# Performance work log

Measured on AMD Instinct MI355X. Metric: run time of the kernel, lower is better.

Reference implementation:

```python
import jax, jax.numpy as jnp
import numpy as np

G, NPG = 2048, 512          # glimpses, points per glimpse
N0 = G * NPG                # 1,048,576 input points
CPG, CPG2 = 128, 32         # clusters per glimpse at level1/level2
M1, M2 = G * CPG, G * CPG2  # 262144, 65536


def _seg_mean_np(x, ids, m):
    cnt = np.bincount(ids, minlength=m).astype(np.float32)
    out = np.stack([np.bincount(ids, weights=x[:, d], minlength=m) for d in range(x.shape[1])], axis=1)
    return (out / np.maximum(cnt, 1.0)[:, None]).astype(np.float32)


def setup_inputs() -> dict:
    key = jax.random.key(0)
    ks = jax.random.split(key, 16)
    rng = np.random.default_rng(0)
    pos_np = (rng.random((N0, 3)) * 4.0).astype(np.float32)
    # voxel_mean_pool level 0: each point -> a cluster within its glimpse
    g_of_pt = np.arange(N0) // NPG
    out_index0 = (g_of_pt * CPG + rng.integers(0, CPG, N0)).astype(np.int64)
    pos1_np = _seg_mean_np(pos_np, out_index0, M1)
    g_of_c1 = np.arange(M1) // CPG
    out_index1 = (g_of_c1 * CPG2 + rng.integers(0, CPG2, M1)).astype(np.int64)
    pos2_np = _seg_mean_np(pos1_np, out_index1, M2)
    out_index2 = (np.arange(M2) // CPG2).astype(np.int64)  # glimpse id per level-2 point

    def w(k, shp, s=0.05):
        return jax.random.normal(k, shp, dtype=jnp.float32) * s

    return {
        "rgb": jax.random.normal(ks[0], (N0, 1), dtype=jnp.float32),
        "pos": jnp.asarray(pos_np), "pos1": jnp.asarray(pos1_np), "pos2": jnp.asarray(pos2_np),
        "out_index0": jnp.asarray(out_index0), "out_index1": jnp.asarray(out_index1),
        "out_index2": jnp.asarray(out_index2),
        "eps": jax.random.normal(ks[1], (G, 128), dtype=jnp.float32),
        # conv1: local (c_in=1 + 3 -> 16), global (16 -> 32)
        "W1l": w(ks[2], (4, 16)), "b1l": jnp.zeros(16), "W1g": w(ks[3], (16, 32)), "b1g": jnp.zeros(32),
        # conv2: (32+3 -> 64), (64 -> 128)
        "W2l": w(ks[4], (35, 64)), "b2l": jnp.zeros(64), "W2g": w(ks[5], (64, 128)), "b2g": jnp.zeros(128),
        # conv3: (128+3 -> 128), (128 -> 256)
        "W3l": w(ks[6], (131, 128)), "b3l": jnp.zeros(128), "W3g": w(ks[7], (128, 256)), "b3g": jnp.zeros(256),
        "Wlin": w(ks[8], (256, 256)), "blin": jnp.zeros(256),
    }


def _point_conv(x_in, pos_in, pos_out, out_index, Wl, bl, Wg, bg):
    # gather relative position of each input point w.r.t. its output center
    rel = pos_in - pos_out[out_index]                      # [E,3]
    h = jax.nn.celu(jnp.concatenate([x_in, rel], -1) @ Wl + bl)  # per-edge MLP
    m = pos_out.shape[0]
    cnt = jax.ops.segment_sum(jnp.ones((h.shape[0],), h.dtype), out_index, num_segments=m)
    agg = jax.ops.segment_sum(h, out_index, num_segments=m) / jnp.maximum(cnt, 1.0)[:, None]
    return agg @ Wg + bg


def reference(rgb, pos, pos1, pos2, out_index0, out_index1, out_index2, eps,
              W1l, b1l, W1g, b1g, W2l, b2l, W2g, b2g, W3l, b3l, W3g, b3g, Wlin, blin):
    f = rgb  # ar=False path: feature = rgb
    f = jax.nn.celu(_point_conv(f, pos, pos1, out_index0, W1l, b1l, W1g, b1g))   # [M1,32]
    f = jax.nn.celu(_point_conv(f, pos1, pos2, out_index1, W2l, b2l, W2g, b2g))  # [M2,128]
    centers = jnp.zeros((G, 3), f.dtype)  # pos_sample = zeros_like(glimpse__center)
    f = jax.nn.celu(_point_conv(f, pos2, centers, out_index2, W3l, b3l, W3g, b3g))  # [G,256]
    out = f @ Wlin + blin
    mu, sg = jnp.split(out, 2, axis=1)
    sigma = jax.nn.softplus(sg)  # to_sigma
    z = mu + sigma * eps         # Normal.rsample
    z_what, z_mask = jnp.split(z, 2, axis=1)
    return z_what, z_mask, mu, sigma, f
```

## Files before the change

kernel.cpp:

```cpp
#include <hip/hip_runtime.h>
#include <hip/hip_bf16.h>
#include <cstddef>

#define G_   2048
#define NPG_ 512
#define CPG_ 128
#define CPG2_ 32
#define N0_  (G_*NPG_)
#define M1_  (G_*CPG_)
#define M2_  (G_*CPG2_)

#define OFF_ZW 0
#define OFF_ZM (G_*64)
#define OFF_MU (2*G_*64)
#define OFF_SG (2*G_*64 + G_*128)
#define OFF_F  (2*G_*64 + 2*G_*128)

typedef __attribute__((ext_vector_type(8))) short bf16x8;
typedef __attribute__((ext_vector_type(4))) float f32x4;

__device__ __forceinline__ float celu_f(float x)     { return x > 0.f ? x : __expf(x) - 1.f; }
__device__ __forceinline__ float softplus_f(float x) { return fmaxf(x, 0.f) + __logf(1.f + __expf(-fabsf(x))); }
__device__ __forceinline__ unsigned short f2bf(float x) {
    __hip_bfloat16 h = __float2bfloat16(x);
    return *reinterpret_cast<unsigned short*>(&h);
}

__global__ __launch_bounds__(256, 6) void k_conv1(
    const float* __restrict__ rgb, const float* __restrict__ pos, const float* __restrict__ pos1,
    const int* __restrict__ idx0, const float* __restrict__ W1l, const float* __restrict__ b1l,
    const float* __restrict__ W1g, const float* __restrict__ b1g, unsigned short* __restrict__ f1,
    const float* __restrict__ W2l, const float* __restrict__ W2g, const float* __restrict__ W3l,
    const float* __restrict__ W3g, const float* __restrict__ Wlin,
    unsigned short* __restrict__ w2lT, unsigned short* __restrict__ w2gT,
    unsigned short* __restrict__ w3lT, unsigned short* __restrict__ w3gT,
    unsigned short* __restrict__ wlinT)
{
    const int g = blockIdx.x, t = threadIdx.x;

    {
        const size_t tid = (size_t)g*256 + t, stride = (size_t)gridDim.x*256;
        for (size_t i = tid; i < 64*64; i += stride) {
            const int ch = i >> 6, k = i & 63;
            w2lT[i] = f2bf(k < 35 ? W2l[k*64 + ch] : 0.f);
        }
        for (size_t i = tid; i < 128*64; i += stride) {
            const int ch = i >> 6, k = i & 63;
            w2gT[i] = f2bf(W2g[k*128 + ch]);
        }
        for (size_t i = tid; i < 128*160; i += stride) {
            const int ch = i / 160, k = i % 160;
            w3lT[i] = f2bf(k < 131 ? W3l[k*128 + ch] : 0.f);
        }
        for (size_t i = tid; i < 256*128; i += stride) {
            const int ch = i >> 7, k = i & 127;
            w3gT[i] = f2bf(W3g[k*256 + ch]);
        }
        for (size_t i = tid; i < 256*256; i += stride) {
            const int ch = i >> 8, k = i & 255;
            wlinT[i] = f2bf(Wlin[k*256 + ch]);
        }
    }

    __shared__ float sx0[NPG_], srx[NPG_], sry[NPG_], srz[NPG_];
    __shared__ unsigned short slc1[NPG_], order[NPG_];
    __shared__ int cnt[CPG_], start[CPG_], ctr[CPG_], scan[CPG_];
    __shared__ float aggT[CPG_*20];
    __shared__ float sW1g[512];

    for (int i = t; i < 512; i += 256) sW1g[i] = W1g[i];
    if (t < CPG_) cnt[t] = 0;
    __syncthreads();

    #pragma unroll
    for (int r = 0; r < 2; r++) {
        const int lp = r*256 + t;
        const int p  = g*NPG_ + lp;
        const int c  = idx0[p];
        const int lc = c - g*CPG_;
        sx0[lp] = rgb[p];
        srx[lp] = pos[p*3+0] - pos1[c*3+0];
        sry[lp] = pos[p*3+1] - pos1[c*3+1];
        srz[lp] = pos[p*3+2] - pos1[c*3+2];
        slc1[lp] = (unsigned short)lc;
        atomicAdd(&cnt[lc], 1);
    }
    __syncthreads();

    if (t < CPG_) {
        int val = cnt[t];
        const int ln = t & 63;
        #pragma unroll
        for (int d = 1; d < 64; d <<= 1) {
            const int v = __shfl_up(val, d, 64);
            if (ln >= d) val += v;
        }
        scan[t] = val;
    }
    __syncthreads();
    if (t >= 64 && t < CPG_) scan[t] += scan[63];
    __syncthreads();
    if (t < CPG_) { const int s = scan[t] - cnt[t]; start[t] = s; ctr[t] = s; }
    __syncthreads();

    #pragma unroll
    for (int r = 0; r < 2; r++) {
        const int lp = r*256 + t;
        const int slot = atomicAdd(&ctr[slc1[lp]], 1);
        order[slot] = (unsigned short)lp;
    }
    __syncthreads();

    {
        const int c = t >> 1, ch0 = (t & 1) * 8;
        float wj[8], wx[8], wy[8], wz[8], bb2[8];
        #pragma unroll
        for (int j = 0; j < 8; j++) {
            wj[j] = W1l[ch0+j]; wx[j] = W1l[16+ch0+j];
            wy[j] = W1l[32+ch0+j]; wz[j] = W1l[48+ch0+j];
            bb2[j] = b1l[ch0+j];
        }
        float a[8];
        #pragma unroll
        for (int j = 0; j < 8; j++) a[j] = 0.f;
        const int n = cnt[c], base = start[c];
        for (int i = 0; i < n; i++) {
            const int lp = order[base + i];
            const float x0 = sx0[lp], rx = srx[lp], ry = sry[lp], rz = srz[lp];
            #pragma unroll
            for (int j = 0; j < 8; j++) {
                const float h = bb2[j] + x0*wj[j] + rx*wx[j] + ry*wy[j] + rz*wz[j];
                a[j] += celu_f(h);
            }
        }
        const float inv = 1.f / fmaxf((float)n, 1.f);
        #pragma unroll
        for (int j = 0; j < 8; j++) aggT[c*20 + ch0 + j] = a[j] * inv;
    }
    __syncthreads();

    const int oc = t & 31;
    float wreg[16];
    #pragma unroll
    for (int j = 0; j < 16; j++) wreg[j] = sW1g[j*32 + oc];
    const float bg = b1g[oc];
    #pragma unroll
    for (int i = 0; i < 16; i++) {
        const int lc = (t >> 5) + i*8;
        float a = bg;
        #pragma unroll
        for (int j = 0; j < 16; j += 4) {
            const float4 a4 = *(const float4*)&aggT[lc*20 + j];
            a += a4.x*wreg[j] + a4.y*wreg[j+1] + a4.z*wreg[j+2] + a4.w*wreg[j+3];
        }
        f1[(size_t)(g*CPG_ + lc)*32 + oc] = f2bf(celu_f(a));
    }
}

__global__ __launch_bounds__(256, 5) void k_conv2(
    const unsigned short* __restrict__ f1, const float* __restrict__ pos1, const float* __restrict__ pos2,
    const int* __restrict__ idx1, const unsigned short* __restrict__ w2lT, const float* __restrict__ b2l,
    const unsigned short* __restrict__ w2gT, const float* __restrict__ b2g, unsigned short* __restrict__ f2)
{
    const int g = blockIdx.x, t = threadIdx.x;
    const int lane = t & 63, wv = t >> 6;
    const int lr = lane & 15, quad = lane >> 4;
    __shared__ __align__(16) unsigned short xs16[CPG_*72];
    __shared__ __align__(16) unsigned short sT[32*136];
    __shared__ int   slc[CPG_];
    __shared__ int   cnti[CPG2_];
    __shared__ float invc[CPG2_];
    unsigned short* const HT   = sT - 0 + 0, *const HT_unused = nullptr;
    unsigned short* const HTp  = xs16;
    unsigned short* const agg2 = sT;

    for (int i = t; i < 1088; i += 256) ((uint2*)sT)[i] = make_uint2(0u, 0u);
    if (t < CPG2_) cnti[t] = 0;
    {
        const uint4 v0 = ((const uint4*)f1)[(size_t)g*512 + t*2];
        const uint4 v1 = ((const uint4*)f1)[(size_t)g*512 + t*2 + 1];
        const int row = t >> 1, col = (t & 1) * 16;
        *(uint4*)&xs16[row*72 + col]     = v0;
        *(uint4*)&xs16[row*72 + col + 8] = v1;
    }
    for (int i = t; i < 128*29; i += 256) {
        const int r = i / 29, c = 35 + (i - r*29);
        xs16[r*72 + c] = 0;
    }
    if (t < CPG_) {
        const int c2 = idx1[g*CPG_ + t];
        slc[t] = c2 - g*CPG2_;
        #pragma unroll
        for (int d = 0; d < 3; d++)
            xs16[t*72 + 32 + d] = f2bf(pos1[(g*CPG_ + t)*3 + d] - pos2[c2*3 + d]);
    }
    __syncthreads();

    float hv[8][4];
    {
        const int chn = wv*16 + lr;
        const bf16x8 bw0 = *(const bf16x8*)&w2lT[chn*64 + quad*8];
        const bf16x8 bw1 = *(const bf16x8*)&w2lT[chn*64 + 32 + quad*8];
        const float bias = b2l[chn];
        #pragma unroll
        for (int m = 0; m < 8; m++) {
            f32x4 acc = (f32x4){bias, bias, bias, bias};
            const bf16x8 a0 = *(const bf16x8*)&xs16[(m*16 + lr)*72 + quad*8];
            const bf16x8 a1 = *(const bf16x8*)&xs16[(m*16 + lr)*72 + 32 + quad*8];
            acc = __builtin_amdgcn_mfma_f32_16x16x32_bf16(a0, bw0, acc, 0, 0, 0);
            acc = __builtin_amdgcn_mfma_f32_16x16x32_bf16(a1, bw1, acc, 0, 0, 0);
            #pragma unroll
            for (int r = 0; r < 4; r++) hv[m][r] = celu_f(acc[r]);
        }
    }
    if (t < CPG_) {
        sT[slc[t]*136 + t] = 0x3F80;
        atomicAdd(&cnti[slc[t]], 1);
    }
    __syncthreads();

    {
        const int chn = wv*16 + lr;
        #pragma unroll
        for (int m = 0; m < 8; m++) {
            uint2 p;
            p.x = (unsigned)f2bf(hv[m][0]) | ((unsigned)f2bf(hv[m][1]) << 16);
            p.y = (unsigned)f2bf(hv[m][2]) | ((unsigned)f2bf(hv[m][3]) << 16);
            *(uint2*)&HTp[chn*136 + m*16 + quad*4] = p;
        }
    }
    if (t < CPG2_) invc[t] = 1.f / fmaxf((float)cnti[t], 1.f);
    __syncthreads();

    float aggv[2][4];
    {
        const int ch = wv*16 + lr;
        f32x4 acc[2];
        acc[0] = (f32x4){0.f, 0.f, 0.f, 0.f};
        acc[1] = (f32x4){0.f, 0.f, 0.f, 0.f};
        #pragma unroll
        for (int ks = 0; ks < 4; ks++) {
            const bf16x8 b = *(const bf16x8*)&HTp[ch*136 + ks*32 + quad*8];
            #pragma unroll
            for (int mt = 0; mt < 2; mt++) {
                const bf16x8 a = *(const bf16x8*)&sT[(mt*16 + lr)*136 + ks*32 + quad*8];
                acc[mt] = __builtin_amdgcn_mfma_f32_16x16x32_bf16(a, b, acc[mt], 0, 0, 0);
            }
        }
        #pragma unroll
        for (int mt = 0; mt < 2; mt++)
        #pragma unroll
        for (int r = 0; r < 4; r++) {
            const int s = mt*16 + quad*4 + r;
            aggv[mt][r] = acc[mt][r] * invc[s];
        }
    }
    __syncthreads();

    {
        const int ch = wv*16 + lr;
        #pragma unroll
        for (int mt = 0; mt < 2; mt++)
        #pragma unroll
        for (int r = 0; r < 4; r++)
            agg2[(mt*16 + quad*4 + r)*72 + ch] = f2bf(aggv[mt][r]);
    }
    __syncthreads();

    {
        f32x4 acc2[2][2];
        int   chn2[2];
        bf16x8 bw[2][2];
        #pragma unroll
        for (int nt = 0; nt < 2; nt++) {
            chn2[nt] = (wv + nt*4)*16 + lr;
            const float bias = b2g[chn2[nt]];
            #pragma unroll
            for (int mt = 0; mt < 2; mt++) acc2[nt][mt] = (f32x4){bias, bias, bias, bias};
            bw[nt][0] = *(const bf16x8*)&w2gT[chn2[nt]*64 + quad*8];
            bw[nt][1] = *(const bf16x8*)&w2gT[chn2[nt]*64 + 32 + quad*8];
        }
        #pragma unroll
        for (int ks = 0; ks < 2; ks++) {
            #pragma unroll
            for (int mt = 0; mt < 2; mt++) {
                const bf16x8 a = *(const bf16x8*)&agg2[(mt*16 + lr)*72 + ks*32 + quad*8];
                acc2[0][mt] = __builtin_amdgcn_mfma_f32_16x16x32_bf16(a, bw[0][ks], acc2[0][mt], 0, 0, 0);
                acc2[1][mt] = __builtin_amdgcn_mfma_f32_16x16x32_bf16(a, bw[1][ks], acc2[1][mt], 0, 0, 0);
            }
        }
        #pragma unroll
        for (int nt = 0; nt < 2; nt++)
        #pragma unroll
        for (int mt = 0; mt < 2; mt++)
        #pragma unroll
        for (int r = 0; r < 4; r++) {
            const int row = mt*16 + quad*4 + r;
            f2[(size_t)(g*CPG2_ + row)*128 + chn2[nt]] = f2bf(celu_f(acc2[nt][mt][r]));
        }
    }
}

__global__ __launch_bounds__(256, 4) void k_conv3(
    const unsigned short* __restrict__ f2, const float* __restrict__ pos2,
    const unsigned short* __restrict__ w3lT, const float* __restrict__ b3l,
    const unsigned short* __restrict__ w3gT, const float* __restrict__ b3g,
    const unsigned short* __restrict__ wlinT, const float* __restrict__ blin,
    const float* __restrict__ eps, float* __restrict__ out)
{
    const int g0 = blockIdx.x * 2, t = threadIdx.x;
    const int lane = t & 63, wv = t >> 6;
    const int lr = lane & 15, quad = lane >> 4;
    __shared__ __align__(16) unsigned short xs16[64*168];
    __shared__ __align__(16) float red2[2*128*9];
    __shared__ __align__(16) unsigned short aggB[16*136];
    __shared__ float outs[512];
    unsigned short* const f3B = (unsigned short*)red2;

    for (int i = t; i < 1088; i += 256) ((unsigned*)aggB)[i] = 0u;
    {
        const int row = t >> 2, q = t & 3;
        const size_t base = (size_t)(g0*CPG2_ + row)*16 + q*4;
        const uint4 v0 = ((const uint4*)f2)[base + 0];
        const uint4 v1 = ((const uint4*)f2)[base + 1];
        const uint4 v2 = ((const uint4*)f2)[base + 2];
        const uint4 v3 = ((const uint4*)f2)[base + 3];
        *(uint4*)&xs16[row*168 + q*32]      = v0;
        *(uint4*)&xs16[row*168 + q*32 + 8]  = v1;
        *(uint4*)&xs16[row*168 + q*32 + 16] = v2;
        *(uint4*)&xs16[row*168 + q*32 + 24] = v3;
    }
    for (int i = t; i < 64*29; i += 256) {
        const int r = i / 29, c = 131 + (i - r*29);
        xs16[r*168 + c] = 0;
    }
    if (t < 64) {
        #pragma unroll
        for (int d = 0; d < 3; d++)
            xs16[t*168 + 128 + d] = f2bf(pos2[(g0*CPG2_ + t)*3 + d]);
    }
    __syncthreads();

    {
        f32x4 acc[2][4];
        int chn[2];
        #pragma unroll
        for (int nt = 0; nt < 2; nt++) {
            chn[nt] = (wv + nt*4)*16 + lr;
            const float bias = b3l[chn[nt]];
            #pragma unroll
            for (int mt = 0; mt < 4; mt++) acc[nt][mt] = (f32x4){bias, bias, bias, bias};
        }
        #pragma unroll
        for (int ks = 0; ks < 5; ks++) {
            const bf16x8 b0 = *(const bf16x8*)&w3lT[chn[0]*160 + ks*32 + quad*8];
            const bf16x8 b1 = *(const bf16x8*)&w3lT[chn[1]*160 + ks*32 + quad*8];
            #pragma unroll
            for (int mt = 0; mt < 4; mt++) {
                const bf16x8 a = *(const bf16x8*)&xs16[(mt*16 + lr)*168 + ks*32 + quad*8];
                acc[0][mt] = __builtin_amdgcn_mfma_f32_16x16x32_bf16(a, b0, acc[0][mt], 0, 0, 0);
                acc[1][mt] = __builtin_amdgcn_mfma_f32_16x16x32_bf16(a, b1, acc[1][mt], 0, 0, 0);
            }
        }
        #pragma unroll
        for (int nt = 0; nt < 2; nt++)
        #pragma unroll
        for (int mt = 0; mt < 4; mt++) {
            float p = celu_f(acc[nt][mt][0]) + celu_f(acc[nt][mt][1])
                    + celu_f(acc[nt][mt][2]) + celu_f(acc[nt][mt][3]);
            const int gl = mt >> 1, pidx = (mt & 1)*4 + quad;
            red2[(gl*128 + chn[nt])*9 + pidx] = p;
        }
    }
    __syncthreads();

    if (t < 256) {
        const int gl = t >> 7, ch = t & 127;
        const float* rp = &red2[(gl*128 + ch)*9];
        float a = 0.f;
        #pragma unroll
        for (int p = 0; p < 8; p++) a += rp[p];
        aggB[gl*136 + ch] = f2bf(a * (1.f/32.f));
    }
    __syncthreads();

    for (int i = t; i < 14*264; i += 256) f3B[2*264 + i] = 0;

    {
        f32x4 c3[4];
        int ch3[4];
        #pragma unroll
        for (int nt = 0; nt < 4; nt++) {
            ch3[nt] = (wv + nt*4)*16 + lr;
            const float bias = b3g[ch3[nt]];
            c3[nt] = (f32x4){bias, bias, bias, bias};
        }
        #pragma unroll
        for (int ks = 0; ks < 4; ks++) {
            const bf16x8 a = *(const bf16x8*)&aggB[lr*136 + ks*32 + quad*8];
            #pragma unroll
            for (int nt = 0; nt < 4; nt++) {
                const bf16x8 b = *(const bf16x8*)&w3gT[ch3[nt]*128 + ks*32 + quad*8];
                c3[nt] = __builtin_amdgcn_mfma_f32_16x16x32_bf16(a, b, c3[nt], 0, 0, 0);
            }
        }
        if (quad == 0) {
            #pragma unroll
            for (int nt = 0; nt < 4; nt++) {
                const float v0 = celu_f(c3[nt][0]);
                const float v1 = celu_f(c3[nt][1]);
                out[OFF_F + (size_t)g0*256 + ch3[nt]]     = v0;
                out[OFF_F + (size_t)(g0+1)*256 + ch3[nt]] = v1;
                f3B[ch3[nt]]       = f2bf(v0);
                f3B[264 + ch3[nt]] = f2bf(v1);
            }
        }
    }
    __syncthreads();

    {
        f32x4 cl[4];
        int ch4[4];
        #pragma unroll
        for (int nt = 0; nt < 4; nt++) {
            ch4[nt] = (wv + nt*4)*16 + lr;
            const float bias = blin[ch4[nt]];
            cl[nt] = (f32x4){bias, bias, bias, bias};
        }
        #pragma unroll
        for (int ks = 0; ks < 8; ks++) {
            const bf16x8 a = *(const bf16x8*)&f3B[lr*264 + ks*32 + quad*8];
            #pragma unroll
            for (int nt = 0; nt < 4; nt++) {
                const bf16x8 b = *(const bf16x8*)&wlinT[ch4[nt]*256 + ks*32 + quad*8];
                cl[nt] = __builtin_amdgcn_mfma_f32_16x16x32_bf16(a, b, cl[nt], 0, 0, 0);
            }
        }
        if (quad == 0) {
            #pragma unroll
            for (int nt = 0; nt < 4; nt++) {
                outs[ch4[nt]]       = cl[nt][0];
                outs[256 + ch4[nt]] = cl[nt][1];
            }
        }
    }
    __syncthreads();

    if (t < 128) {
        #pragma unroll
        for (int gl = 0; gl < 2; gl++) {
            const int g = g0 + gl;
            const float mu    = outs[gl*256 + t];
            const float sigma = softplus_f(outs[gl*256 + 128 + t]);
            const float z     = mu + sigma * eps[g*128 + t];
            out[OFF_MU + g*128 + t] = mu;
            out[OFF_SG + g*128 + t] = sigma;
            if (t < 64) out[OFF_ZW + g*64 + t] = z;
            else        out[OFF_ZM + g*64 + (t - 64)] = z;
        }
    }
}

extern "C" void kernel_launch(void* const* d_in, const int* in_sizes, int n_in,
                              void* d_out, int out_size, void* d_ws, size_t ws_size,
                              hipStream_t stream)
{
    const float* rgb  = (const float*)d_in[0];
    const float* pos  = (const float*)d_in[1];
    const float* pos1 = (const float*)d_in[2];
    const float* pos2 = (const float*)d_in[3];
    const int*   idx0 = (const int*)d_in[4];
    const int*   idx1 = (const int*)d_in[5];
    const float* eps  = (const float*)d_in[7];
    const float* W1l = (const float*)d_in[8],  *b1l = (const float*)d_in[9];
    const float* W1g = (const float*)d_in[10], *b1g = (const float*)d_in[11];
    const float* W2l = (const float*)d_in[12], *b2l = (const float*)d_in[13];
    const float* W2g = (const float*)d_in[14], *b2g = (const float*)d_in[15];
    const float* W3l = (const float*)d_in[16], *b3l = (const float*)d_in[17];
    const float* W3g = (const float*)d_in[18], *b3g = (const float*)d_in[19];
    const float* Wlin = (const float*)d_in[20], *blin = (const float*)d_in[21];

    unsigned short* f1    = (unsigned short*)d_ws;
    unsigned short* f2    = f1 + (size_t)M1_*32;
    unsigned short* w2lT  = f2 + (size_t)M2_*128;
    unsigned short* w2gT  = w2lT + 64*64;
    unsigned short* w3lT  = w2gT + 128*64;
    unsigned short* w3gT  = w3lT + 128*160;
    unsigned short* wlinT = w3gT + 256*128;
    float* outp = (float*)d_out;

    k_conv1<<<G_,   256, 0, stream>>>(rgb, pos, pos1, idx0, W1l, b1l, W1g, b1g, f1,
                                      W2l, W2g, W3l, W3g, Wlin,
                                      w2lT, w2gT, w3lT, w3gT, wlinT);
    k_conv2<<<G_,   256, 0, stream>>>(f1, pos1, pos2, idx1, w2lT, b2l, w2gT, b2g, f2);
    k_conv3<<<G_/2, 256, 0, stream>>>(f2, pos2, w3lT, b3l, w3gT, b3g, wlinT, blin, eps, outp);
}
```

Before: 177.3 us.

## Fuse three conv stages into one per-glimpse kernel with shared-memory intermediates

Merges conv1, conv2 and conv3+head into a single kernel in which each block handles one glimpse, so the level-1 and level-2 features stay in a time-multiplexed shared-memory buffer instead of round-tripping through global workspace. Weight transposition moves into a separate small prep kernel. Conv3 now runs one glimpse per block rather than two, which halves its MFMA tile reuse. The larger shared footprint also lowers the occupancy bound to 3 blocks per CU.

```diff
diff --git a/kernel.cpp b/kernel.cpp
--- a/kernel.cpp
+++ b/kernel.cpp
@@ -6,9 +6,6 @@
 #define NPG_ 512
 #define CPG_ 128
 #define CPG2_ 32
-#define N0_  (G_*NPG_)
-#define M1_  (G_*CPG_)
-#define M2_  (G_*CPG2_)
 
 #define OFF_ZW 0
 #define OFF_ZM (G_*64)
@@ -26,50 +23,93 @@
     return *reinterpret_cast<unsigned short*>(&h);
 }
 
-__global__ __launch_bounds__(256, 6) void k_conv1(
+__global__ void k_prep(const float* __restrict__ W2l, const float* __restrict__ W2g,
+                       const float* __restrict__ W3l, const float* __restrict__ W3g,
+                       const float* __restrict__ Wlin,
+                       unsigned short* __restrict__ w2lT, unsigned short* __restrict__ w2gT,
+                       unsigned short* __restrict__ w3lT, unsigned short* __restrict__ w3gT,
+                       unsigned short* __restrict__ wlinT)
+{
+    const int tid = blockIdx.x*256 + threadIdx.x, stride = gridDim.x*256;
+    for (int i = tid; i < 64*64; i += stride) {
+        const int ch = i >> 6, k = i & 63;
+        w2lT[i] = f2bf(k < 35 ? W2l[k*64 + ch] : 0.f);
+    }
+    for (int i = tid; i < 128*64; i += stride) {
+        const int ch = i >> 6, k = i & 63;
+        w2gT[i] = f2bf(W2g[k*128 + ch]);
+    }
+    for (int i = tid; i < 128*160; i += stride) {
+        const int ch = i / 160, k = i % 160;
+        w3lT[i] = f2bf(k < 131 ? W3l[k*128 + ch] : 0.f);
+    }
+    for (int i = tid; i < 256*128; i += stride) {
+        const int ch = i >> 7, k = i & 127;
+        w3gT[i] = f2bf(W3g[k*256 + ch]);
+    }
+    for (int i = tid; i < 256*256; i += stride) {
+        const int ch = i >> 8, k = i & 255;
+        wlinT[i] = f2bf(Wlin[k*256 + ch]);
+    }
+}
+
+__global__ __launch_bounds__(256, 3) void k_fused(
     const float* __restrict__ rgb, const float* __restrict__ pos, const float* __restrict__ pos1,
-    const int* __restrict__ idx0, const float* __restrict__ W1l, const float* __restrict__ b1l,
-    const float* __restrict__ W1g, const float* __restrict__ b1g, unsigned short* __restrict__ f1,
-    const float* __restrict__ W2l, const float* __restrict__ W2g, const float* __restrict__ W3l,
-    const float* __restrict__ W3g, const float* __restrict__ Wlin,
-    unsigned short* __restrict__ w2lT, unsigned short* __restrict__ w2gT,
-    unsigned short* __restrict__ w3lT, unsigned short* __restrict__ w3gT,
-    unsigned short* __restrict__ wlinT)
+    const float* __restrict__ pos2, const int* __restrict__ idx0, const int* __restrict__ idx1,
+    const float* __restrict__ eps,
+    const float* __restrict__ W1l, const float* __restrict__ b1l,
+    const float* __restrict__ W1g, const float* __restrict__ b1g,
+    const unsigned short* __restrict__ w2lT, const float* __restrict__ b2l,
+    const unsigned short* __restrict__ w2gT, const float* __restrict__ b2g,
+    const unsigned short* __restrict__ w3lT, const float* __restrict__ b3l,
+    const unsigned short* __restrict__ w3gT, const float* __restrict__ b3g,
+    const unsigned short* __restrict__ wlinT, const float* __restrict__ blin,
+    float* __restrict__ out)
 {
     const int g = blockIdx.x, t = threadIdx.x;
-
-    {
-        const size_t tid = (size_t)g*256 + t, stride = (size_t)gridDim.x*256;
-        for (size_t i = tid; i < 64*64; i += stride) {
-            const int ch = i >> 6, k = i & 63;
-            w2lT[i] = f2bf(k < 35 ? W2l[k*64 + ch] : 0.f);
-        }
-        for (size_t i = tid; i < 128*64; i += stride) {
-            const int ch = i >> 6, k = i & 63;
-            w2gT[i] = f2bf(W2g[k*128 + ch]);
-        }
-        for (size_t i = tid; i < 128*160; i += stride) {
-            const int ch = i / 160, k = i % 160;
-            w3lT[i] = f2bf(k < 131 ? W3l[k*128 + ch] : 0.f);
-        }
-        for (size_t i = tid; i < 256*128; i += stride) {
-            const int ch = i >> 7, k = i & 127;
-            w3gT[i] = f2bf(W3g[k*256 + ch]);
-        }
-        for (size_t i = tid; i < 256*256; i += stride) {
-            const int ch = i >> 8, k = i & 255;
-            wlinT[i] = f2bf(Wlin[k*256 + ch]);
-        }
-    }
-
-    __shared__ float sx0[NPG_], srx[NPG_], sry[NPG_], srz[NPG_];
-    __shared__ unsigned short slc1[NPG_], order[NPG_];
-    __shared__ int cnt[CPG_], start[CPG_], ctr[CPG_], scan[CPG_];
-    __shared__ float aggT[CPG_*20];
-    __shared__ float sW1g[512];
+    const int lane = t & 63, wv = t >> 6;
+    const int lr = lane & 15, quad = lane >> 4;
+
+    __shared__ __align__(16) unsigned char smem[44800];
+    float* const sx0 = (float*)(smem);
+    float* const srx = sx0 + 512;
+    float* const sry = srx + 512;
+    float* const srz = sry + 512;
+    unsigned short* const slc1  = (unsigned short*)(smem + 8192);
+    unsigned short* const order = slc1 + 512;
+    unsigned short* const sT    = (unsigned short*)smem;
+    unsigned short* const agg2  = (unsigned short*)smem;
+    float* const red  = (float*)smem;
+    unsigned short* const aggB = (unsigned short*)(smem + 4608);
+    float* const aggT = (float*)(smem + 10240);
+    float* const sW1g = (float*)(smem + 20480);
+    unsigned short* const xs3  = (unsigned short*)(smem + 10240);
+    unsigned short* const f3B  = (unsigned short*)(smem + 10240);
+    unsigned short* const xs16 = (unsigned short*)(smem + 22528);
+    unsigned short* const HT   = xs16;
+    int* const cnt   = (int*)(smem + 40960);
+    int* const start = cnt + 128;
+    int* const ctr   = start + 128;
+    int* const scan  = ctr + 128;
+    int* const slc   = (int*)(smem + 43008);
+    int* const cnti  = (int*)(smem + 43520);
+    float* const invc = (float*)(smem + 43648);
+    float* const outs = (float*)(smem + 43776);
 
     for (int i = t; i < 512; i += 256) sW1g[i] = W1g[i];
     if (t < CPG_) cnt[t] = 0;
+    if (t < CPG2_) cnti[t] = 0;
+    if (t < CPG_) {
+        const int c2 = idx1[g*CPG_ + t];
+        slc[t] = c2 - g*CPG2_;
+        #pragma unroll
+        for (int d = 0; d < 3; d++)
+            xs16[t*72 + 32 + d] = f2bf(pos1[(g*CPG_ + t)*3 + d] - pos2[c2*3 + d]);
+    }
+    for (int i = t; i < 128*29; i += 256) {
+        const int r = i / 29, c = 35 + (i - r*29);
+        xs16[r*72 + c] = 0;
+    }
     __syncthreads();
 
     #pragma unroll
@@ -85,6 +125,7 @@
         slc1[lp] = (unsigned short)lc;
         atomicAdd(&cnt[lc], 1);
     }
+    if (t < CPG_) atomicAdd(&cnti[slc[t]], 1);
     __syncthreads();
 
     if (t < CPG_) {
@@ -101,6 +142,7 @@
     if (t >= 64 && t < CPG_) scan[t] += scan[63];
     __syncthreads();
     if (t < CPG_) { const int s = scan[t] - cnt[t]; start[t] = s; ctr[t] = s; }
+    if (t < CPG2_) invc[t] = 1.f / fmaxf((float)cnti[t], 1.f);
     __syncthreads();
 
     #pragma unroll
@@ -139,61 +181,27 @@
     }
     __syncthreads();
 
-    const int oc = t & 31;
-    float wreg[16];
-    #pragma unroll
-    for (int j = 0; j < 16; j++) wreg[j] = sW1g[j*32 + oc];
-    const float bg = b1g[oc];
-    #pragma unroll
-    for (int i = 0; i < 16; i++) {
-        const int lc = (t >> 5) + i*8;
-        float a = bg;
-        #pragma unroll
-        for (int j = 0; j < 16; j += 4) {
-            const float4 a4 = *(const float4*)&aggT[lc*20 + j];
-            a += a4.x*wreg[j] + a4.y*wreg[j+1] + a4.z*wreg[j+2] + a4.w*wreg[j+3];
-        }
-        f1[(size_t)(g*CPG_ + lc)*32 + oc] = f2bf(celu_f(a));
-    }
-}
-
-__global__ __launch_bounds__(256, 5) void k_conv2(
-    const unsigned short* __restrict__ f1, const float* __restrict__ pos1, const float* __restrict__ pos2,
-    const int* __restrict__ idx1, const unsigned short* __restrict__ w2lT, const float* __restrict__ b2l,
-    const unsigned short* __restrict__ w2gT, const float* __restrict__ b2g, unsigned short* __restrict__ f2)
-{
-    const int g = blockIdx.x, t = threadIdx.x;
-    const int lane = t & 63, wv = t >> 6;
-    const int lr = lane & 15, quad = lane >> 4;
-    __shared__ __align__(16) unsigned short xs16[CPG_*72];
-    __shared__ __align__(16) unsigned short sT[32*136];
-    __shared__ int   slc[CPG_];
-    __shared__ int   cnti[CPG2_];
-    __shared__ float invc[CPG2_];
-    unsigned short* const HT   = sT - 0 + 0, *const HT_unused = nullptr;
-    unsigned short* const HTp  = xs16;
-    unsigned short* const agg2 = sT;
-
+    {
+        const int oc = t & 31;
+        float wreg[16];
+        #pragma unroll
+        for (int j = 0; j < 16; j++) wreg[j] = sW1g[j*32 + oc];
+        const float bg = b1g[oc];
+        #pragma unroll
+        for (int i = 0; i < 16; i++) {
+            const int lc = (t >> 5) + i*8;
+            float a = bg;
+            #pragma unroll
+            for (int j = 0; j < 16; j += 4) {
+                const float4 a4 = *(const float4*)&aggT[lc*20 + j];
+                a += a4.x*wreg[j] + a4.y*wreg[j+1] + a4.z*wreg[j+2] + a4.w*wreg[j+3];
+            }
+            xs16[lc*72 + oc] = f2bf(celu_f(a));
+        }
+    }
     for (int i = t; i < 1088; i += 256) ((uint2*)sT)[i] = make_uint2(0u, 0u);
-    if (t < CPG2_) cnti[t] = 0;
-    {
-        const uint4 v0 = ((const uint4*)f1)[(size_t)g*512 + t*2];
-        const uint4 v1 = ((const uint4*)f1)[(size_t)g*512 + t*2 + 1];
-        const int row = t >> 1, col = (t & 1) * 16;
-        *(uint4*)&xs16[row*72 + col]     = v0;
-        *(uint4*)&xs16[row*72 + col + 8] = v1;
-    }
-    for (int i = t; i < 128*29; i += 256) {
-        const int r = i / 29, c = 35 + (i - r*29);
-        xs16[r*72 + c] = 0;
-    }
-    if (t < CPG_) {
-        const int c2 = idx1[g*CPG_ + t];
-        slc[t] = c2 - g*CPG2_;
-        #pragma unroll
-        for (int d = 0; d < 3; d++)
-            xs16[t*72 + 32 + d] = f2bf(pos1[(g*CPG_ + t)*3 + d] - pos2[c2*3 + d]);
-    }
+    __syncthreads();
+    if (t < CPG_) sT[slc[t]*136 + t] = 0x3F80;
     __syncthreads();
 
     float hv[8][4];
@@ -213,10 +221,6 @@
             for (int r = 0; r < 4; r++) hv[m][r] = celu_f(acc[r]);
         }
     }
-    if (t < CPG_) {
-        sT[slc[t]*136 + t] = 0x3F80;
-        atomicAdd(&cnti[slc[t]], 1);
-    }
     __syncthreads();
 
     {
@@ -226,10 +230,18 @@
             uint2 p;
             p.x = (unsigned)f2bf(hv[m][0]) | ((unsigned)f2bf(hv[m][1]) << 16);
             p.y = (unsigned)f2bf(hv[m][2]) | ((unsigned)f2bf(hv[m][3]) << 16);
-            *(uint2*)&HTp[chn*136 + m*16 + quad*4] = p;
-        }
-    }
-    if (t < CPG2_) invc[t] = 1.f / fmaxf((float)cnti[t], 1.f);
+            *(uint2*)&HT[chn*136 + m*16 + quad*4] = p;
+        }
+    }
+    if (t < CPG2_) {
+        #pragma unroll
+        for (int d = 0; d < 3; d++)
+            xs3[t*168 + 128 + d] = f2bf(pos2[(g*CPG2_ + t)*3 + d]);
+    }
+    for (int i = t; i < 32*29; i += 256) {
+        const int r = i / 29, c = 131 + (i - r*29);
+        xs3[r*168 + c] = 0;
+    }
     __syncthreads();
 
     float aggv[2][4];
@@ -240,7 +252,7 @@
         acc[1] = (f32x4){0.f, 0.f, 0.f, 0.f};
         #pragma unroll
         for (int ks = 0; ks < 4; ks++) {
-            const bf16x8 b = *(const bf16x8*)&HTp[ch*136 + ks*32 + quad*8];
+            const bf16x8 b = *(const bf16x8*)&HT[ch*136 + ks*32 + quad*8];
             #pragma unroll
             for (int mt = 0; mt < 2; mt++) {
                 const bf16x8 a = *(const bf16x8*)&sT[(mt*16 + lr)*136 + ks*32 + quad*8];
@@ -250,10 +262,8 @@
         #pragma unroll
         for (int mt = 0; mt < 2; mt++)
         #pragma unroll
-        for (int r = 0; r < 4; r++) {
-            const int s = mt*16 + quad*4 + r;
-            aggv[mt][r] = acc[mt][r] * invc[s];
-        }
+        for (int r = 0; r < 4; r++)
+            aggv[mt][r] = acc[mt][r] * invc[mt*16 + quad*4 + r];
     }
     __syncthreads();
 
@@ -296,68 +306,29 @@
         #pragma unroll
         for (int r = 0; r < 4; r++) {
             const int row = mt*16 + quad*4 + r;
-            f2[(size_t)(g*CPG2_ + row)*128 + chn2[nt]] = f2bf(celu_f(acc2[nt][mt][r]));
-        }
-    }
-}
-
-__global__ __launch_bounds__(256, 4) void k_conv3(
-    const unsigned short* __restrict__ f2, const float* __restrict__ pos2,
-    const unsigned short* __restrict__ w3lT, const float* __restrict__ b3l,
-    const unsigned short* __restrict__ w3gT, const float* __restrict__ b3g,
-    const unsigned short* __restrict__ wlinT, const float* __restrict__ blin,
-    const float* __restrict__ eps, float* __restrict__ out)
-{
-    const int g0 = blockIdx.x * 2, t = threadIdx.x;
-    const int lane = t & 63, wv = t >> 6;
-    const int lr = lane & 15, quad = lane >> 4;
-    __shared__ __align__(16) unsigned short xs16[64*168];
-    __shared__ __align__(16) float red2[2*128*9];
-    __shared__ __align__(16) unsigned short aggB[16*136];
-    __shared__ float outs[512];
-    unsigned short* const f3B = (unsigned short*)red2;
+            xs3[row*168 + chn2[nt]] = f2bf(celu_f(acc2[nt][mt][r]));
+        }
+    }
+    __syncthreads();
 
     for (int i = t; i < 1088; i += 256) ((unsigned*)aggB)[i] = 0u;
     {
-        const int row = t >> 2, q = t & 3;
-        const size_t base = (size_t)(g0*CPG2_ + row)*16 + q*4;
-        const uint4 v0 = ((const uint4*)f2)[base + 0];
-        const uint4 v1 = ((const uint4*)f2)[base + 1];
-        const uint4 v2 = ((const uint4*)f2)[base + 2];
-        const uint4 v3 = ((const uint4*)f2)[base + 3];
-        *(uint4*)&xs16[row*168 + q*32]      = v0;
-        *(uint4*)&xs16[row*168 + q*32 + 8]  = v1;
-        *(uint4*)&xs16[row*168 + q*32 + 16] = v2;
-        *(uint4*)&xs16[row*168 + q*32 + 24] = v3;
-    }
-    for (int i = t; i < 64*29; i += 256) {
-        const int r = i / 29, c = 131 + (i - r*29);
-        xs16[r*168 + c] = 0;
-    }
-    if (t < 64) {
-        #pragma unroll
-        for (int d = 0; d < 3; d++)
-            xs16[t*168 + 128 + d] = f2bf(pos2[(g0*CPG2_ + t)*3 + d]);
-    }
-    __syncthreads();
-
-    {
-        f32x4 acc[2][4];
+        f32x4 acc[2][2];
         int chn[2];
         #pragma unroll
         for (int nt = 0; nt < 2; nt++) {
             chn[nt] = (wv + nt*4)*16 + lr;
             const float bias = b3l[chn[nt]];
             #pragma unroll
-            for (int mt = 0; mt < 4; mt++) acc[nt][mt] = (f32x4){bias, bias, bias, bias};
+            for (int mt = 0; mt < 2; mt++) acc[nt][mt] = (f32x4){bias, bias, bias, bias};
         }
         #pragma unroll
         for (int ks = 0; ks < 5; ks++) {
             const bf16x8 b0 = *(const bf16x8*)&w3lT[chn[0]*160 + ks*32 + quad*8];
             const bf16x8 b1 = *(const bf16x8*)&w3lT[chn[1]*160 + ks*32 + quad*8];
             #pragma unroll
-            for (int mt = 0; mt < 4; mt++) {
-                const bf16x8 a = *(const bf16x8*)&xs16[(mt*16 + lr)*168 + ks*32 + quad*8];
+            for (int mt = 0; mt < 2; mt++) {
+                const bf16x8 a = *(const bf16x8*)&xs3[(mt*16 + lr)*168 + ks*32 + quad*8];
                 acc[0][mt] = __builtin_amdgcn_mfma_f32_16x16x32_bf16(a, b0, acc[0][mt], 0, 0, 0);
                 acc[1][mt] = __builtin_amdgcn_mfma_f32_16x16x32_bf16(a, b1, acc[1][mt], 0, 0, 0);
             }
@@ -365,26 +336,23 @@
         #pragma unroll
         for (int nt = 0; nt < 2; nt++)
         #pragma unroll
-        for (int mt = 0; mt < 4; mt++) {
-            float p = celu_f(acc[nt][mt][0]) + celu_f(acc[nt][mt][1])
-                    + celu_f(acc[nt][mt][2]) + celu_f(acc[nt][mt][3]);
-            const int gl = mt >> 1, pidx = (mt & 1)*4 + quad;
-            red2[(gl*128 + chn[nt])*9 + pidx] = p;
-        }
-    }
-    __syncthreads();
-
-    if (t < 256) {
-        const int gl = t >> 7, ch = t & 127;
-        const float* rp = &red2[(gl*128 + ch)*9];
+        for (int mt = 0; mt < 2; mt++) {
+            const float p = celu_f(acc[nt][mt][0]) + celu_f(acc[nt][mt][1])
+                          + celu_f(acc[nt][mt][2]) + celu_f(acc[nt][mt][3]);
+            red[chn[nt]*9 + mt*4 + quad] = p;
+        }
+    }
+    __syncthreads();
+
+    if (t < 128) {
+        const float* rp = &red[t*9];
         float a = 0.f;
         #pragma unroll
         for (int p = 0; p < 8; p++) a += rp[p];
-        aggB[gl*136 + ch] = f2bf(a * (1.f/32.f));
-    }
-    __syncthreads();
-
-    for (int i = t; i < 14*264; i += 256) f3B[2*264 + i] = 0;
+        aggB[t] = f2bf(a * (1.f/32.f));
+    }
+    for (int i = t; i < 15*264; i += 256) f3B[264 + i] = 0;
+    __syncthreads();
 
     {
         f32x4 c3[4];
@@ -407,12 +375,9 @@
         if (quad == 0) {
             #pragma unroll
             for (int nt = 0; nt < 4; nt++) {
-                const float v0 = celu_f(c3[nt][0]);
-                const float v1 = celu_f(c3[nt][1]);
-                out[OFF_F + (size_t)g0*256 + ch3[nt]]     = v0;
-                out[OFF_F + (size_t)(g0+1)*256 + ch3[nt]] = v1;
-                f3B[ch3[nt]]       = f2bf(v0);
-                f3B[264 + ch3[nt]] = f2bf(v1);
+                const float v = celu_f(c3[nt][0]);
+                out[OFF_F + (size_t)g*256 + ch3[nt]] = v;
+                f3B[ch3[nt]] = f2bf(v);
             }
         }
     }
@@ -438,26 +403,19 @@
         }
         if (quad == 0) {
             #pragma unroll
-            for (int nt = 0; nt < 4; nt++) {
-                outs[ch4[nt]]       = cl[nt][0];
-                outs[256 + ch4[nt]] = cl[nt][1];
-            }
+            for (int nt = 0; nt < 4; nt++) outs[ch4[nt]] = cl[nt][0];
         }
     }
     __syncthreads();
 
     if (t < 128) {
-        #pragma unroll
-        for (int gl = 0; gl < 2; gl++) {
-            const int g = g0 + gl;
-            const float mu    = outs[gl*256 + t];
-            const float sigma = softplus_f(outs[gl*256 + 128 + t]);
-            const float z     = mu + sigma * eps[g*128 + t];
-            out[OFF_MU + g*128 + t] = mu;
-            out[OFF_SG + g*128 + t] = sigma;
-            if (t < 64) out[OFF_ZW + g*64 + t] = z;
-            else        out[OFF_ZM + g*64 + (t - 64)] = z;
-        }
+        const float mu    = outs[t];
+        const float sigma = softplus_f(outs[128 + t]);
+        const float z     = mu + sigma * eps[g*128 + t];
+        out[OFF_MU + g*128 + t] = mu;
+        out[OFF_SG + g*128 + t] = sigma;
+        if (t < 64) out[OFF_ZW + g*64 + t] = z;
+        else        out[OFF_ZM + g*64 + (t - 64)] = z;
     }
 }
 
@@ -480,18 +438,16 @@
     const float* W3g = (const float*)d_in[18], *b3g = (const float*)d_in[19];
     const float* Wlin = (const float*)d_in[20], *blin = (const float*)d_in[21];
 
-    unsigned short* f1    = (unsigned short*)d_ws;
-    unsigned short* f2    = f1 + (size_t)M1_*32;
-    unsigned short* w2lT  = f2 + (size_t)M2_*128;
+    unsigned short* w2lT  = (unsigned short*)d_ws;
     unsigned short* w2gT  = w2lT + 64*64;
     unsigned short* w3lT  = w2gT + 128*64;
     unsigned short* w3gT  = w3lT + 128*160;
     unsigned short* wlinT = w3gT + 256*128;
     float* outp = (float*)d_out;
 
-    k_conv1<<<G_,   256, 0, stream>>>(rgb, pos, pos1, idx0, W1l, b1l, W1g, b1g, f1,
-                                      W2l, W2g, W3l, W3g, Wlin,
-                                      w2lT, w2gT, w3lT, w3gT, wlinT);
-    k_conv2<<<G_,   256, 0, stream>>>(f1, pos1, pos2, idx1, w2lT, b2l, w2gT, b2g, f2);
-    k_conv3<<<G_/2, 256, 0, stream>>>(f2, pos2, w3lT, b3l, w3gT, b3g, wlinT, blin, eps, outp);
+    k_prep <<<64, 256, 0, stream>>>(W2l, W2g, W3l, W3g, Wlin, w2lT, w2gT, w3lT, w3gT, wlinT);
+    k_fused<<<G_, 256, 0, stream>>>(rgb, pos, pos1, pos2, idx0, idx1, eps,
+                                    W1l, b1l, W1g, b1g,
+                                    w2lT, b2l, w2gT, b2g, w3lT, b3l, w3gT, b3g, wlinT, blin,
+                                    outp);
 }
```

New measurement: 197.4 us. 1.11x slower.
